# Kernel optimization log

Hardware: AMD Instinct MI355X
Metric: run time of the kernel (lower is better)

Reference implementation:

```python
import jax, jax.numpy as jnp
import numpy as np
import math

B, T, C = 4, 2048, 1024
D_ATTN, N_HEAD = 1024, 16
HEAD = D_ATTN // N_HEAD


def setup_inputs() -> dict:
    key = jax.random.key(0)
    k1, k2, k3 = jax.random.split(key, 3)
    x = jax.random.normal(k1, (B, T, C), dtype=jnp.float32)
    mask = jnp.tril(jnp.ones((T, T), dtype=jnp.int32))  # causal mask, 0 = blocked
    W_qkv = jax.random.normal(k2, (C, 3 * D_ATTN), dtype=jnp.float32) * (1.0 / math.sqrt(C))
    b_qkv = jnp.zeros((3 * D_ATTN,), dtype=jnp.float32)
    W_out = jax.random.normal(k3, (D_ATTN, C), dtype=jnp.float32) * (1.0 / math.sqrt(D_ATTN))
    b_out = jnp.zeros((C,), dtype=jnp.float32)
    return {"x": x, "mask": mask, "W_qkv": W_qkv, "b_qkv": b_qkv, "W_out": W_out, "b_out": b_out}


def reference(x, mask, W_qkv, b_qkv, W_out, b_out):
    Bx, Tx, Cx = x.shape
    qkv = x @ W_qkv + b_qkv                      # [B, T, 3*d_attn]
    q, k, v = jnp.split(qkv, 3, axis=-1)
    # [B, T, d_attn] -> [B, H, T, head]
    q = q.reshape(Bx, Tx, N_HEAD, HEAD).transpose(0, 2, 1, 3)
    k = k.reshape(Bx, Tx, N_HEAD, HEAD).transpose(0, 2, 1, 3)
    v = v.reshape(Bx, Tx, N_HEAD, HEAD).transpose(0, 2, 1, 3)
    scale = 1.0 / math.sqrt(HEAD)
    scores = jnp.einsum('bhqd,bhkd->bhqk', q, k) * scale  # [B, H, T, T]
    scores = jnp.where(mask == 0, -jnp.inf, scores)
    att = jax.nn.softmax(scores, axis=-1)
    out = jnp.einsum('bhqk,bhkd->bhqd', att, v)           # [B, H, T, head]
    out = out.transpose(0, 2, 1, 3).reshape(Bx, Tx, D_ATTN)
    return out @ W_out + b_out
```

## Files before the change

### kernel.cpp

```cpp
#include <hip/hip_runtime.h>

#define B_    4
#define T_    2048
#define C_    1024
#define DATTN 1024
#define NHEAD 16
#define M_    (B_*T_)
#define NQKV  (3*DATTN)

typedef __bf16 bf16;
typedef bf16  bf16x8 __attribute__((ext_vector_type(8)));
typedef bf16  bf16x4 __attribute__((ext_vector_type(4)));
typedef short s16x4  __attribute__((ext_vector_type(4)));
typedef float f32x4  __attribute__((ext_vector_type(4)));
typedef unsigned short u16x8 __attribute__((ext_vector_type(8)));

#define NEGBIG (-1e30f)

typedef const __attribute__((address_space(1))) unsigned int* gas_u32;
typedef __attribute__((address_space(3))) unsigned int* las_u32;

static __device__ __forceinline__ f32x4 mfma16(bf16x4 a, bf16x4 b, f32x4 c) {
#if __has_builtin(__builtin_amdgcn_mfma_f32_16x16x16bf16_1k)
    return __builtin_amdgcn_mfma_f32_16x16x16bf16_1k(
        __builtin_bit_cast(s16x4, a), __builtin_bit_cast(s16x4, b), c, 0, 0, 0);
#else
    asm("v_mfma_f32_16x16x16_bf16 %0, %1, %2, %0" : "+v"(c) : "v"(a), "v"(b));
    return c;
#endif
}

static __device__ __forceinline__ bf16x4 pk4(float a, float b, float c, float d) {
    union { unsigned int u[2]; bf16x4 v; } r;
    asm("v_cvt_pk_bf16_f32 %0, %1, %2" : "=v"(r.u[0]) : "v"(a), "v"(b));
    asm("v_cvt_pk_bf16_f32 %0, %1, %2" : "=v"(r.u[1]) : "v"(c), "v"(d));
    return r.v;
}

__global__ void detect_dtype(const unsigned short* __restrict__ x, int* flag) {
    __shared__ int cnt;
    if (threadIdx.x == 0) cnt = 0;
    __syncthreads();
    int local = 0;
    for (int j = 0; j < 8; ++j) {
        u16x8 v = *(const u16x8*)&x[(j * 256 + threadIdx.x) * 8];
        for (int k = 0; k < 8; ++k)
            if ((v[k] & 0x7F80) == 0x7F80) ++local;
    }
    atomicAdd(&cnt, local);
    __syncthreads();
    if (threadIdx.x == 0) *flag = (cnt > 0) ? 1 : 0;
}

__global__ void convert_x_any(const void* __restrict__ src, bf16* __restrict__ dst,
                              int n, const int* __restrict__ flag) {
    int i = (blockIdx.x * 256 + threadIdx.x) * 8;
    if (i >= n) return;
    if (*flag == 0) {
        *(bf16x8*)&dst[i] = *(const bf16x8*)((const bf16*)src + i);
    } else {
        const float* s = (const float*)src + i;
        f32x4 a = *(const f32x4*)s, b2 = *(const f32x4*)(s + 4);
        bf16x8 r;
        r[0] = (bf16)a[0]; r[1] = (bf16)a[1]; r[2] = (bf16)a[2]; r[3] = (bf16)a[3];
        r[4] = (bf16)b2[0]; r[5] = (bf16)b2[1]; r[6] = (bf16)b2[2]; r[7] = (bf16)b2[3];
        *(bf16x8*)&dst[i] = r;
    }
}

__global__ void prep_bias(const void* __restrict__ bq, const void* __restrict__ bo,
                          bf16* __restrict__ dq, bf16* __restrict__ do_,
                          const int* __restrict__ flag) {
    const int f = *flag;
    int i = blockIdx.x * 256 + threadIdx.x;
    if (i < NQKV)
        dq[i] = f ? (bf16)((const float*)bq)[i] : ((const bf16*)bq)[i];
    else if (i - NQKV < C_)
        do_[i - NQKV] = f ? (bf16)((const float*)bo)[i - NQKV] : ((const bf16*)bo)[i - NQKV];
}

__global__ void transpose_w_any(const void* __restrict__ src, bf16* __restrict__ dst,
                                int R, int C, const int* __restrict__ flag) {
    __shared__ bf16 tile[32][33];
    const int f = *flag;
    const int c0 = blockIdx.x * 32, r0 = blockIdx.y * 32;
    const int tx = threadIdx.x & 31, ty = threadIdx.x >> 5;
    for (int p = 0; p < 4; ++p) {
        int row = p * 8 + ty;
        size_t idx = (size_t)(r0 + row) * C + c0 + tx;
        float v = f ? ((const float*)src)[idx] : (float)((const bf16*)src)[idx];
        tile[row][tx] = (bf16)v;
    }
    __syncthreads();
    for (int p = 0; p < 4; ++p) {
        int row = p * 8 + ty;
        dst[(size_t)(c0 + row) * R + r0 + tx] = tile[tx][row];
    }
}

__global__ void transpose_v(const bf16* __restrict__ qkv, bf16* __restrict__ vt) {
    __shared__ bf16 tile[32][33];
    const int t0 = blockIdx.x * 32, d0 = blockIdx.y * 32, bh = blockIdx.z;
    const int b = bh >> 4, h = bh & 15;
    const int tx = threadIdx.x & 31, ty = threadIdx.x >> 5;
    for (int p = 0; p < 4; ++p) {
        int tt = p * 8 + ty;
        tile[tt][tx] = qkv[((size_t)b * T_ + t0 + tt) * NQKV + 2 * DATTN + h * 64 + d0 + tx];
    }
    __syncthreads();
    for (int p = 0; p < 4; ++p) {
        int dd = p * 8 + ty;
        vt[((size_t)bh * 64 + d0 + dd) * T_ + t0 + tx] = tile[tx][dd];
    }
}

template<typename TC>
__global__ __launch_bounds__(256) void gemm_bt(const bf16* __restrict__ A,
                                               const bf16* __restrict__ Bt,
                                               const bf16* __restrict__ bias,
                                               TC* __restrict__ Cc,
                                               int M, int N, int K,
                                               const int* __restrict__ flag, int want) {
    if (flag && *flag != want) return;
    __shared__ __align__(16) bf16 As[128 * 64];
    __shared__ __align__(16) bf16 Bs[128 * 64];
    const int tid  = threadIdx.x;
    const int lane = tid & 63, wave = tid >> 6;
    const int quad = lane >> 4, l15 = lane & 15;
    const int wr = wave >> 1, wc = wave & 1;
    const int m0 = blockIdx.y * 128, n0 = blockIdx.x * 128;
    const int srow = lane >> 3;
    const int scol = ((lane & 7) ^ srow) * 8;
    const int l7x8 = (l15 & 7);

    f32x4 acc[4][4];
    for (int i = 0; i < 4; ++i)
        for (int j = 0; j < 4; ++j)
            acc[i][j] = f32x4{0.f, 0.f, 0.f, 0.f};

    for (int k0 = 0; k0 < K; k0 += 64) {
        for (int c = 0; c < 4; ++c) {
            int chunk = wave * 4 + c;
            int row = chunk * 8 + srow;
            __builtin_amdgcn_global_load_lds(
                (gas_u32)&A[(size_t)(m0 + row) * K + k0 + scol],
                (las_u32)&As[chunk * 512], 16, 0, 0);
            __builtin_amdgcn_global_load_lds(
                (gas_u32)&Bt[(size_t)(n0 + row) * K + k0 + scol],
                (las_u32)&Bs[chunk * 512], 16, 0, 0);
        }
        __syncthreads();
        for (int ks = 0; ks < 2; ++ks) {
            bf16x8 af[4], bfr[4];
            for (int i = 0; i < 4; ++i)
                af[i] = *(const bf16x8*)&As[(wr * 64 + i * 16 + l15) * 64 +
                                            (((ks * 4 + quad) ^ l7x8) * 8)];
            for (int j = 0; j < 4; ++j)
                bfr[j] = *(const bf16x8*)&Bs[(wc * 64 + j * 16 + l15) * 64 +
                                             (((ks * 4 + quad) ^ l7x8) * 8)];
            for (int i = 0; i < 4; ++i)
                for (int j = 0; j < 4; ++j)
                    acc[i][j] = __builtin_amdgcn_mfma_f32_16x16x32_bf16(af[i], bfr[j], acc[i][j], 0, 0, 0);
        }
        __syncthreads();
    }

    for (int i = 0; i < 4; ++i) {
        int row = m0 + wr * 64 + i * 16 + quad * 4;
        for (int j = 0; j < 4; ++j) {
            int col = n0 + wc * 64 + j * 16 + l15;
            float bv = (float)bias[col];
            for (int r = 0; r < 4; ++r) {
                float v = acc[i][j][r] + bv;
                if constexpr (__is_same(TC, float)) Cc[(size_t)(row + r) * N + col] = v;
                else                                Cc[(size_t)(row + r) * N + col] = (bf16)v;
            }
        }
    }
}

__global__ __launch_bounds__(256, 4) void attn_fused7(const bf16* __restrict__ qkv,
                                                      const bf16* __restrict__ vt,
                                                      bf16* __restrict__ out) {
    __shared__ __align__(16) bf16 Ks[2][64 * 64];
    __shared__ __align__(16) bf16 Vs[2][64 * 64];
    const int tid  = threadIdx.x;
    const int lane = tid & 63, wave = tid >> 6;
    const int quad = lane >> 4, l15 = lane & 15;
    const int srow = lane >> 3;
    const int scol = ((lane & 7) ^ srow) * 8;
    const int l7   = l15 & 7;
    const int g0   = quad >> 1, h4 = (quad & 1) * 4;
    const int bh = blockIdx.x & 63;
    const int i  = blockIdx.x >> 6;
    const int b  = bh >> 4, h = bh & 15;
    const int lo = i, hi = 31 - i;
    const size_t rowbase = (size_t)b * T_;
    const float SC = 0.125f * 1.44269504088896f;

    auto stage = [&](int kt, int buf) {
        const int k0 = kt * 64;
        for (int p = 0; p < 2; ++p) {
            int chunk = wave * 2 + p;
            int row = chunk * 8 + srow;
            __builtin_amdgcn_global_load_lds(
                (gas_u32)&qkv[(rowbase + k0 + row) * NQKV + DATTN + h * 64 + scol],
                (las_u32)&Ks[buf][chunk * 512], 16, 0, 0);
            __builtin_amdgcn_global_load_lds(
                (gas_u32)&vt[((size_t)bh * 64 + row) * T_ + k0 + scol],
                (las_u32)&Vs[buf][chunk * 512], 16, 0, 0);
        }
    };

    bf16x8 qf[2][2];
#pragma unroll
    for (int t = 0; t < 2; ++t) {
        int q0 = (t ? hi : lo) * 64;
        size_t r = rowbase + q0 + wave * 16 + l15;
        const bf16* p = &qkv[r * NQKV + h * 64];
        qf[t][0] = *(const bf16x8*)&p[quad * 8];
        qf[t][1] = *(const bf16x8*)&p[32 + quad * 8];
    }

    f32x4 oa[2][4];
    float lacc[2] = {0.f, 0.f};
#pragma unroll
    for (int t = 0; t < 2; ++t)
        for (int c = 0; c < 4; ++c)
            oa[t][c] = f32x4{0.f, 0.f, 0.f, 0.f};

    stage(0, 0);

    for (int kt = 0; kt <= hi; ++kt) {
        const int k0 = kt * 64;
        const bool act0 = (kt <= lo);
        const int buf = kt & 1;
        __syncthreads();
        if (kt < hi) stage(kt + 1, buf ^ 1);

        const bf16* Kb = Ks[buf];
        const bf16* Vb = Vs[buf];

        f32x4 s0[4], s1[4];
#pragma unroll
        for (int c = 0; c < 4; ++c) {
            s0[c] = f32x4{0.f, 0.f, 0.f, 0.f};
            s1[c] = f32x4{0.f, 0.f, 0.f, 0.f};
        }
#pragma unroll
        for (int ks = 0; ks < 2; ++ks)
#pragma unroll
            for (int c = 0; c < 4; ++c) {
                bf16x8 kf = *(const bf16x8*)&Kb[(c * 16 + l15) * 64 +
                                                (((ks * 4 + quad) ^ l7) * 8)];
                if (act0) s0[c] = __builtin_amdgcn_mfma_f32_16x16x32_bf16(kf, qf[0][ks], s0[c], 0, 0, 0);
                s1[c] = __builtin_amdgcn_mfma_f32_16x16x32_bf16(kf, qf[1][ks], s1[c], 0, 0, 0);
            }

        bf16x4 paf[2][4];
#pragma unroll
        for (int t = 0; t < 2; ++t) {
            if (t == 0 && !act0) continue;
            const int q0 = (t ? hi : lo) * 64;
            const bool diag = (kt == (t ? hi : lo));
            const int qa = q0 + wave * 16 + l15;
            float lsum = 0.f;
#pragma unroll
            for (int c = 0; c < 4; ++c) {
                const int keyb = k0 + c * 16 + quad * 4;
                float pr[4];
#pragma unroll
                for (int r = 0; r < 4; ++r) {
                    float v = (t ? s1[c][r] : s0[c][r]) * SC;
                    if (diag && keyb + r > qa) v = NEGBIG;
                    float p = __builtin_amdgcn_exp2f(v);
                    lsum += p;
                    pr[r] = p;
                }
                paf[t][c] = pk4(pr[0], pr[1], pr[2], pr[3]);
            }
            lacc[t] += lsum;
        }

#pragma unroll
        for (int c = 0; c < 4; ++c)
#pragma unroll
            for (int c2 = 0; c2 < 4; ++c2) {
                bf16x4 vf = *(const bf16x4*)&Vb[(c2 * 16 + l15) * 64 +
                                                (((2 * c + g0) ^ l7) * 8) + h4];
                if (act0) oa[0][c2] = mfma16(paf[0][c], vf, oa[0][c2]);
                oa[1][c2] = mfma16(paf[1][c], vf, oa[1][c2]);
            }
    }

#pragma unroll
    for (int t = 0; t < 2; ++t) {
        int q0 = (t ? hi : lo) * 64;
        float tot = lacc[t];
        tot += __shfl_xor(tot, 16);
        tot += __shfl_xor(tot, 32);
        float inv[4];
#pragma unroll
        for (int r = 0; r < 4; ++r) inv[r] = 1.f / __shfl(tot, quad * 4 + r);
        size_t r0 = rowbase + q0 + wave * 16 + quad * 4;
#pragma unroll
        for (int c2 = 0; c2 < 4; ++c2) {
            int col = h * 64 + c2 * 16 + l15;
#pragma unroll
            for (int r = 0; r < 4; ++r)
                out[(r0 + r) * (size_t)DATTN + col] = (bf16)(oa[t][c2][r] * inv[r]);
        }
    }
}

extern "C" void kernel_launch(void* const* d_in, const int* in_sizes, int n_in,
                              void* d_out, int out_size, void* d_ws, size_t ws_size,
                              hipStream_t stream) {
    const void* x     = d_in[0];
    const void* W_qkv = d_in[2];
    const void* b_qkv = d_in[3];
    const void* W_out = d_in[4];
    const void* b_out = d_in[5];

    char* ws = (char*)d_ws;
    int*  flag    = (int*)ws;
    bf16* qkv_buf = (bf16*)(ws + 256);
    bf16* Wqkv_t  = (bf16*)(ws + 256 + 50331648);
    bf16* Wout_t  = (bf16*)(ws + 256 + 56623104);
    bf16* att_buf = (bf16*)(ws + 256 + 58720256);
    bf16* vt_buf  = (bf16*)(ws + 256 + 75497472);
    bf16* x_bf    = (bf16*)(ws + 256 + 92274688);
    bf16* bq_bf   = (bf16*)(ws + 256 + 109051904);
    bf16* bo_bf   = (bf16*)(ws + 256 + 109058048);

    detect_dtype<<<1, 256, 0, stream>>>((const unsigned short*)x, flag);

    convert_x_any<<<M_ * C_ / (256 * 8), 256, 0, stream>>>(x, x_bf, M_ * C_, flag);
    prep_bias<<<(NQKV + C_) / 256, 256, 0, stream>>>(b_qkv, b_out, bq_bf, bo_bf, flag);
    transpose_w_any<<<dim3(NQKV / 32, C_ / 32), 256, 0, stream>>>(W_qkv, Wqkv_t, C_, NQKV, flag);
    transpose_w_any<<<dim3(C_ / 32, DATTN / 32), 256, 0, stream>>>(W_out, Wout_t, DATTN, C_, flag);

    gemm_bt<bf16><<<dim3(NQKV / 128, M_ / 128), 256, 0, stream>>>(
        x_bf, Wqkv_t, bq_bf, qkv_buf, M_, NQKV, C_, nullptr, 0);

    transpose_v<<<dim3(T_ / 32, 2, B_ * NHEAD), 256, 0, stream>>>(qkv_buf, vt_buf);

    attn_fused7<<<dim3(B_ * NHEAD * 16), 256, 0, stream>>>(qkv_buf, vt_buf, att_buf);

    gemm_bt<bf16 ><<<dim3(C_ / 128, M_ / 128), 256, 0, stream>>>(
        att_buf, Wout_t, bo_bf, (bf16*)d_out, M_, C_, DATTN, flag, 0);
    gemm_bt<float><<<dim3(C_ / 128, M_ / 128), 256, 0, stream>>>(
        att_buf, Wout_t, bo_bf, (float*)d_out, M_, C_, DATTN, flag, 1);
}
```

Baseline: 280.0 us.

## Fold softmax scale into Q weights and compute row sums via MFMA

The softmax scale (1/sqrt(head)·log2e) is pre-multiplied into the Q columns of the QKV weight and bias during preprocessing, so the attention inner loop no longer scales each score. Row sums of probabilities are now accumulated with extra MFMAs against a ones vector, replacing scalar adds and the final cross-lane shuffles. K/V staging addresses are computed incrementally from running pointers to cut per-iteration index math. Trade-offs: the scaled Q is rounded to bf16 after scaling, and the extra MFMAs add matrix-unit work; the row sums are also taken from bf16-rounded probabilities.

After: 282.9 us. Within noise of the previous version (+1.0%).

```diff
diff --git a/kernel.cpp b/kernel.cpp
--- a/kernel.cpp
+++ b/kernel.cpp
@@ -16,6 +16,7 @@
 typedef unsigned short u16x8 __attribute__((ext_vector_type(8)));
 
 #define NEGBIG (-1e30f)
+#define QSCALE (0.125f * 1.44269504088896f)
 
 typedef const __attribute__((address_space(1))) unsigned int* gas_u32;
 typedef __attribute__((address_space(3))) unsigned int* las_u32;
@@ -73,23 +74,28 @@
                           const int* __restrict__ flag) {
     const int f = *flag;
     int i = blockIdx.x * 256 + threadIdx.x;
-    if (i < NQKV)
-        dq[i] = f ? (bf16)((const float*)bq)[i] : ((const bf16*)bq)[i];
-    else if (i - NQKV < C_)
+    if (i < NQKV) {
+        float v = f ? ((const float*)bq)[i] : (float)((const bf16*)bq)[i];
+        if (i < DATTN) v *= QSCALE;
+        dq[i] = (bf16)v;
+    } else if (i - NQKV < C_) {
         do_[i - NQKV] = f ? (bf16)((const float*)bo)[i - NQKV] : ((const bf16*)bo)[i - NQKV];
+    }
 }
 
 __global__ void transpose_w_any(const void* __restrict__ src, bf16* __restrict__ dst,
-                                int R, int C, const int* __restrict__ flag) {
+                                int R, int C, const int* __restrict__ flag,
+                                float scale, int scale_cols) {
     __shared__ bf16 tile[32][33];
     const int f = *flag;
     const int c0 = blockIdx.x * 32, r0 = blockIdx.y * 32;
     const int tx = threadIdx.x & 31, ty = threadIdx.x >> 5;
+    const float s = (c0 + tx < scale_cols) ? scale : 1.0f;
     for (int p = 0; p < 4; ++p) {
         int row = p * 8 + ty;
         size_t idx = (size_t)(r0 + row) * C + c0 + tx;
         float v = f ? ((const float*)src)[idx] : (float)((const bf16*)src)[idx];
-        tile[row][tx] = (bf16)v;
+        tile[row][tx] = (bf16)(v * s);
     }
     __syncthreads();
     for (int p = 0; p < 4; ++p) {
@@ -179,7 +185,7 @@
     }
 }
 
-__global__ __launch_bounds__(256, 4) void attn_fused7(const bf16* __restrict__ qkv,
+__global__ __launch_bounds__(256, 4) void attn_fused8(const bf16* __restrict__ qkv,
                                                       const bf16* __restrict__ vt,
                                                       bf16* __restrict__ out) {
     __shared__ __align__(16) bf16 Ks[2][64 * 64];
@@ -196,18 +202,20 @@
     const int b  = bh >> 4, h = bh & 15;
     const int lo = i, hi = 31 - i;
     const size_t rowbase = (size_t)b * T_;
-    const float SC = 0.125f * 1.44269504088896f;
-
-    auto stage = [&](int kt, int buf) {
-        const int k0 = kt * 64;
+
+    const size_t koff = (size_t)(wave * 16 + srow) * NQKV + scol;
+    const size_t voff = (size_t)(wave * 16 + srow) * T_ + scol;
+    const bf16* kp = qkv + rowbase * NQKV + DATTN + h * 64;
+    const bf16* vp = vt + (size_t)bh * 64 * T_;
+
+    auto stage = [&](const bf16* kq, const bf16* vq, int buf) {
         for (int p = 0; p < 2; ++p) {
             int chunk = wave * 2 + p;
-            int row = chunk * 8 + srow;
             __builtin_amdgcn_global_load_lds(
-                (gas_u32)&qkv[(rowbase + k0 + row) * NQKV + DATTN + h * 64 + scol],
+                (gas_u32)(kq + koff + (size_t)p * 8 * NQKV),
                 (las_u32)&Ks[buf][chunk * 512], 16, 0, 0);
             __builtin_amdgcn_global_load_lds(
-                (gas_u32)&vt[((size_t)bh * 64 + row) * T_ + k0 + scol],
+                (gas_u32)(vq + voff + (size_t)p * 8 * T_),
                 (las_u32)&Vs[buf][chunk * 512], 16, 0, 0);
         }
     };
@@ -222,21 +230,33 @@
         qf[t][1] = *(const bf16x8*)&p[32 + quad * 8];
     }
 
+    bf16x4 onesf;
+#pragma unroll
+    for (int j = 0; j < 4; ++j) onesf[j] = (bf16)1.0f;
+
     f32x4 oa[2][4];
-    float lacc[2] = {0.f, 0.f};
-#pragma unroll
-    for (int t = 0; t < 2; ++t)
+    f32x4 lac[2];
+#pragma unroll
+    for (int t = 0; t < 2; ++t) {
+        lac[t] = f32x4{0.f, 0.f, 0.f, 0.f};
         for (int c = 0; c < 4; ++c)
             oa[t][c] = f32x4{0.f, 0.f, 0.f, 0.f};
-
-    stage(0, 0);
+    }
+
+    stage(kp, vp, 0);
+    kp += (size_t)64 * NQKV;
+    vp += 64;
 
     for (int kt = 0; kt <= hi; ++kt) {
         const int k0 = kt * 64;
         const bool act0 = (kt <= lo);
         const int buf = kt & 1;
         __syncthreads();
-        if (kt < hi) stage(kt + 1, buf ^ 1);
+        if (kt < hi) {
+            stage(kp, vp, buf ^ 1);
+            kp += (size_t)64 * NQKV;
+            vp += 64;
+        }
 
         const bf16* Kb = Ks[buf];
         const bf16* Vb = Vs[buf];
@@ -264,22 +284,24 @@
             const int q0 = (t ? hi : lo) * 64;
             const bool diag = (kt == (t ? hi : lo));
             const int qa = q0 + wave * 16 + l15;
-            float lsum = 0.f;
 #pragma unroll
             for (int c = 0; c < 4; ++c) {
                 const int keyb = k0 + c * 16 + quad * 4;
                 float pr[4];
 #pragma unroll
                 for (int r = 0; r < 4; ++r) {
-                    float v = (t ? s1[c][r] : s0[c][r]) * SC;
+                    float v = t ? s1[c][r] : s0[c][r];
                     if (diag && keyb + r > qa) v = NEGBIG;
-                    float p = __builtin_amdgcn_exp2f(v);
-                    lsum += p;
-                    pr[r] = p;
+                    pr[r] = __builtin_amdgcn_exp2f(v);
                 }
                 paf[t][c] = pk4(pr[0], pr[1], pr[2], pr[3]);
             }
-            lacc[t] += lsum;
+        }
+
+#pragma unroll
+        for (int c = 0; c < 4; ++c) {
+            if (act0) lac[0] = mfma16(paf[0][c], onesf, lac[0]);
+            lac[1] = mfma16(paf[1][c], onesf, lac[1]);
         }
 
 #pragma unroll
@@ -296,12 +318,9 @@
 #pragma unroll
     for (int t = 0; t < 2; ++t) {
         int q0 = (t ? hi : lo) * 64;
-        float tot = lacc[t];
-        tot += __shfl_xor(tot, 16);
-        tot += __shfl_xor(tot, 32);
         float inv[4];
 #pragma unroll
-        for (int r = 0; r < 4; ++r) inv[r] = 1.f / __shfl(tot, quad * 4 + r);
+        for (int r = 0; r < 4; ++r) inv[r] = 1.f / lac[t][r];
         size_t r0 = rowbase + q0 + wave * 16 + quad * 4;
 #pragma unroll
         for (int c2 = 0; c2 < 4; ++c2) {
@@ -337,15 +356,17 @@
 
     convert_x_any<<<M_ * C_ / (256 * 8), 256, 0, stream>>>(x, x_bf, M_ * C_, flag);
     prep_bias<<<(NQKV + C_) / 256, 256, 0, stream>>>(b_qkv, b_out, bq_bf, bo_bf, flag);
-    transpose_w_any<<<dim3(NQKV / 32, C_ / 32), 256, 0, stream>>>(W_qkv, Wqkv_t, C_, NQKV, flag);
-    transpose_w_any<<<dim3(C_ / 32, DATTN / 32), 256, 0, stream>>>(W_out, Wout_t, DATTN, C_, flag);
+    transpose_w_any<<<dim3(NQKV / 32, C_ / 32), 256, 0, stream>>>(
+        W_qkv, Wqkv_t, C_, NQKV, flag, QSCALE, DATTN);
+    transpose_w_any<<<dim3(C_ / 32, DATTN / 32), 256, 0, stream>>>(
+        W_out, Wout_t, DATTN, C_, flag, 1.0f, 0);
 
     gemm_bt<bf16><<<dim3(NQKV / 128, M_ / 128), 256, 0, stream>>>(
         x_bf, Wqkv_t, bq_bf, qkv_buf, M_, NQKV, C_, nullptr, 0);
 
     transpose_v<<<dim3(T_ / 32, 2, B_ * NHEAD), 256, 0, stream>>>(qkv_buf, vt_buf);
 
-    attn_fused7<<<dim3(B_ * NHEAD * 16), 256, 0, stream>>>(qkv_buf, vt_buf, att_buf);
+    attn_fused8<<<dim3(B_ * NHEAD * 16), 256, 0, stream>>>(qkv_buf, vt_buf, att_buf);
 
     gemm_bt<bf16 ><<<dim3(C_ / 128, M_ / 128), 256, 0, stream>>>(
         att_buf, Wout_t, bo_bf, (bf16*)d_out, M_, C_, DATTN, flag, 0);
```
